# Kernel optimization log

Measured on AMD Instinct MI355X. Metric: run time of the kernel, lower is better.

## Reference

```python
import jax, jax.numpy as jnp
import numpy as np

# snntorch Leaky defaults / CFG constants
BETA = 0.9      # CFG.lif_beta
IAPP = 0.0      # CFG.Iapp
THR = 1.0       # snn.Leaky default threshold
SLOPE = 25.0    # surrogate.fast_sigmoid default slope


@jax.custom_vjp
def spike(x):
    # Heaviside spike with fast-sigmoid surrogate gradient
    return (x > 0).astype(x.dtype)

def _spike_fwd(x):
    return spike(x), x

def _spike_bwd(x, g):
    return (g / (SLOPE * jnp.abs(x) + 1.0) ** 2,)

spike.defvjp(_spike_fwd, _spike_bwd)


def setup_inputs() -> dict:
    key = jax.random.key(0)
    z = jax.random.normal(key, (32, 1024, 512), dtype=jnp.float32)
    return {"z": z}


def reference(z):
    # z: [B, T, H]; sequential LIF over time axis.
    # snntorch Leaky (reset='subtract'):
    #   reset = detach(V_prev > thr)
    #   V_k   = beta * V_prev + input_k - reset * thr
    #   spk_k = heaviside(V_k - thr)
    # Original loop: input at step k is z[:, k-1] + Iapp (noise std = 0.0).
    B, T, H = z.shape
    zt = jnp.transpose(z[:, :-1, :], (1, 0, 2))  # [T-1, B, H]
    V0 = jnp.zeros((B, H), dtype=z.dtype)

    def step(V, zin):
        reset = jax.lax.stop_gradient((V > THR).astype(V.dtype))
        Vn = BETA * V + (zin + IAPP) - reset * THR
        spk = spike(Vn - THR)
        return Vn, spk

    _, spks = jax.lax.scan(step, V0, zt)  # spks: [T-1, B, H]
    # T[:, 0, :] stays zero (loop starts at k=1)
    Tout = jnp.concatenate(
        [jnp.zeros((B, 1, H), dtype=z.dtype), jnp.transpose(spks, (1, 0, 2))],
        axis=1,
    )
    return Tout
```

## Files before the change

### kernel.cpp

```cpp
#include <hip/hip_runtime.h>


#define LIF_H 512
#define LIF_C 31

__global__ __launch_bounds__(64, 1) void lif_kernel(const float* __restrict__ z,
                                                    float* __restrict__ out) {
    const int n = blockIdx.x * 64 + threadIdx.x;
    const int b = n >> 9;
    const int h = n & (LIF_H - 1);
    const int base = b * (1024 * LIF_H) + h;

    const float* zp = z + base;
    float* op = out + base + LIF_H;

    out[base] = 0.0f;

    float bufA[LIF_C], bufB[LIF_C];
    float V = 0.0f;

#pragma unroll
    for (int i = 0; i < LIF_C; ++i) bufA[i] = zp[i * LIF_H];
    __builtin_amdgcn_sched_barrier(0);

    for (int p = 0; p < 16; ++p) {
        const int c0 = 2 * p;

#pragma unroll
        for (int i = 0; i < LIF_C; ++i)
            bufB[i] = zp[((c0 + 1) * LIF_C + i) * LIF_H];
        __builtin_amdgcn_sched_barrier(0);

#pragma unroll
        for (int i = 0; i < LIF_C; ++i) {
            const int s = c0 * LIF_C + i;
            const float v0 = __fadd_rn(__fmul_rn(0.9f, V), bufA[i]);
            const float Vn = (V > 1.0f) ? __fsub_rn(v0, 1.0f) : v0;
            op[s * LIF_H] = (Vn > 1.0f) ? 1.0f : 0.0f;
            V = Vn;
        }
        __builtin_amdgcn_sched_barrier(0);

#pragma unroll
        for (int i = 0; i < LIF_C; ++i)
            bufA[i] = zp[((c0 + 2) * LIF_C + i) * LIF_H];
        __builtin_amdgcn_sched_barrier(0);

#pragma unroll
        for (int i = 0; i < LIF_C; ++i) {
            const int s = (c0 + 1) * LIF_C + i;
            const float v0 = __fadd_rn(__fmul_rn(0.9f, V), bufB[i]);
            const float Vn = (V > 1.0f) ? __fsub_rn(v0, 1.0f) : v0;
            op[s * LIF_H] = (Vn > 1.0f) ? 1.0f : 0.0f;
            V = Vn;
        }
        __builtin_amdgcn_sched_barrier(0);
    }

#pragma unroll
    for (int i = 0; i < LIF_C; ++i) {
        const int s = 32 * LIF_C + i;
        const float v0 = __fadd_rn(__fmul_rn(0.9f, V), bufA[i]);
        const float Vn = (V > 1.0f) ? __fsub_rn(v0, 1.0f) : v0;
        op[s * LIF_H] = (Vn > 1.0f) ? 1.0f : 0.0f;
        V = Vn;
    }
}

extern "C" void kernel_launch(void* const* d_in, const int* in_sizes, int n_in,
                              void* d_out, int out_size, void* d_ws, size_t ws_size,
                              hipStream_t stream) {
    const float* z = (const float*)d_in[0];
    float* out = (float*)d_out;
    dim3 block(64);
    dim3 grid((32 * LIF_H) / 64);
    hipLaunchKernelGGL(lif_kernel, grid, block, 0, stream, z, out);
}
```

Before: 117.0 us.

## Add producer waves streaming input into double-buffered LDS via global_load_lds

Each block now has four producer waves that copy 128-timestep chunks of the input into a double-buffered LDS tile using direct global-to-LDS loads, plus one consumer wave that runs the sequential LIF recurrence from LDS. This is meant to take global-load latency off the serial dependency chain and replace strided per-lane loads with wide 16-byte loads. Block barriers at each chunk keep producers and consumer in step. The cost is a barrier per chunk and extra waves per block, while the grid stays at 256 blocks of one compute wave each.

```diff
diff --git a/kernel.cpp b/kernel.cpp
--- a/kernel.cpp
+++ b/kernel.cpp
@@ -2,68 +2,101 @@
 
 
 #define LIF_H 512
-#define LIF_C 31
+#define LIF_T 1024
+#define CH 128
+#define NCH 8
+#define NPROD 4
+#define NTHREADS (64 * (1 + NPROD))
 
-__global__ __launch_bounds__(64, 1) void lif_kernel(const float* __restrict__ z,
-                                                    float* __restrict__ out) {
-    const int n = blockIdx.x * 64 + threadIdx.x;
-    const int b = n >> 9;
-    const int h = n & (LIF_H - 1);
-    const int base = b * (1024 * LIF_H) + h;
+__global__ __launch_bounds__(NTHREADS, 1) void lif_kernel(const float* __restrict__ z,
+                                                          float* __restrict__ out) {
+    __shared__ float lds[2][CH * 64];
 
-    const float* zp = z + base;
-    float* op = out + base + LIF_H;
+    const int tid  = threadIdx.x;
+    const int wave = tid >> 6;
+    const int lane = tid & 63;
+    const int bid  = blockIdx.x;
+    const int b    = bid >> 3;
+    const int h0   = (bid & 7) << 6;
 
-    out[base] = 0.0f;
+    const float* zb = z   + b * (LIF_T * LIF_H) + h0;
+    float*       ob = out + b * (LIF_T * LIF_H) + h0;
 
-    float bufA[LIF_C], bufB[LIF_C];
+    if (wave == 0) {
+        ob[lane] = 0.0f;
+    } else {
+        const int p = wave - 1;
+#pragma unroll
+        for (int j = 0; j < 8; ++j) {
+            const int r0 = p * 32 + j * 4;
+            const float* g = zb + (r0 + (lane >> 4)) * LIF_H + (lane & 15) * 4;
+            __builtin_amdgcn_global_load_lds(
+                (__attribute__((address_space(1))) void*)g,
+                (__attribute__((address_space(3))) void*)&lds[0][r0 * 64],
+                16, 0, 0);
+        }
+        asm volatile("s_waitcnt vmcnt(0)" ::: "memory");
+    }
+    asm volatile("" ::: "memory");
+    __builtin_amdgcn_s_barrier();
+    asm volatile("" ::: "memory");
+
     float V = 0.0f;
 
+    for (int c = 0; c < NCH; ++c) {
+        const int cur = c & 1;
+
+        if (wave > 0) {
+            if (c + 1 < NCH) {
+                const int p = wave - 1;
 #pragma unroll
-    for (int i = 0; i < LIF_C; ++i) bufA[i] = zp[i * LIF_H];
-    __builtin_amdgcn_sched_barrier(0);
+                for (int j = 0; j < 8; ++j) {
+                    const int r0 = p * 32 + j * 4;
+                    const float* g = zb + ((c + 1) * CH + r0 + (lane >> 4)) * LIF_H
+                                        + (lane & 15) * 4;
+                    __builtin_amdgcn_global_load_lds(
+                        (__attribute__((address_space(1))) void*)g,
+                        (__attribute__((address_space(3))) void*)&lds[cur ^ 1][r0 * 64],
+                        16, 0, 0);
+                }
+                asm volatile("s_waitcnt vmcnt(0)" ::: "memory");
+            }
+        } else {
+            const float* lb = &lds[cur][0];
+            const bool lastc = (c == NCH - 1);
+#pragma unroll 1
+            for (int sub = 0; sub < 4; ++sub) {
+                float rb[32];
+#pragma unroll
+                for (int i = 0; i < 32; ++i)
+                    rb[i] = lb[(sub * 32 + i) * 64 + lane];
+                __builtin_amdgcn_sched_barrier(0);
 
-    for (int p = 0; p < 16; ++p) {
-        const int c0 = 2 * p;
+                const int s0 = c * CH + sub * 32;
+                if (!lastc || sub < 3) {
+#pragma unroll
+                    for (int i = 0; i < 32; ++i) {
+                        const float v0 = __fadd_rn(__fmul_rn(0.9f, V), rb[i]);
+                        const float Vn = (V > 1.0f) ? __fsub_rn(v0, 1.0f) : v0;
+                        ob[(s0 + i + 1) * LIF_H + lane] = (Vn > 1.0f) ? 1.0f : 0.0f;
+                        V = Vn;
+                    }
+                } else {
+#pragma unroll
+                    for (int i = 0; i < 31; ++i) {
+                        const float v0 = __fadd_rn(__fmul_rn(0.9f, V), rb[i]);
+                        const float Vn = (V > 1.0f) ? __fsub_rn(v0, 1.0f) : v0;
+                        ob[(s0 + i + 1) * LIF_H + lane] = (Vn > 1.0f) ? 1.0f : 0.0f;
+                        V = Vn;
+                    }
+                }
+                __builtin_amdgcn_sched_barrier(0);
+            }
+        }
 
-#pragma unroll
-        for (int i = 0; i < LIF_C; ++i)
-            bufB[i] = zp[((c0 + 1) * LIF_C + i) * LIF_H];
-        __builtin_amdgcn_sched_barrier(0);
-
-#pragma unroll
-        for (int i = 0; i < LIF_C; ++i) {
-            const int s = c0 * LIF_C + i;
-            const float v0 = __fadd_rn(__fmul_rn(0.9f, V), bufA[i]);
-            const float Vn = (V > 1.0f) ? __fsub_rn(v0, 1.0f) : v0;
-            op[s * LIF_H] = (Vn > 1.0f) ? 1.0f : 0.0f;
-            V = Vn;
-        }
-        __builtin_amdgcn_sched_barrier(0);
-
-#pragma unroll
-        for (int i = 0; i < LIF_C; ++i)
-            bufA[i] = zp[((c0 + 2) * LIF_C + i) * LIF_H];
-        __builtin_amdgcn_sched_barrier(0);
-
-#pragma unroll
-        for (int i = 0; i < LIF_C; ++i) {
-            const int s = (c0 + 1) * LIF_C + i;
-            const float v0 = __fadd_rn(__fmul_rn(0.9f, V), bufB[i]);
-            const float Vn = (V > 1.0f) ? __fsub_rn(v0, 1.0f) : v0;
-            op[s * LIF_H] = (Vn > 1.0f) ? 1.0f : 0.0f;
-            V = Vn;
-        }
-        __builtin_amdgcn_sched_barrier(0);
-    }
-
-#pragma unroll
-    for (int i = 0; i < LIF_C; ++i) {
-        const int s = 32 * LIF_C + i;
-        const float v0 = __fadd_rn(__fmul_rn(0.9f, V), bufA[i]);
-        const float Vn = (V > 1.0f) ? __fsub_rn(v0, 1.0f) : v0;
-        op[s * LIF_H] = (Vn > 1.0f) ? 1.0f : 0.0f;
-        V = Vn;
+        asm volatile("" ::: "memory");
+        __builtin_amdgcn_s_barrier();
+        asm volatile("" ::: "memory");
     }
 }
 
@@ -72,7 +105,5 @@
                               hipStream_t stream) {
     const float* z = (const float*)d_in[0];
     float* out = (float*)d_out;
-    dim3 block(64);
-    dim3 grid((32 * LIF_H) / 64);
-    hipLaunchKernelGGL(lif_kernel, grid, block, 0, stream, z, out);
+    hipLaunchKernelGGL(lif_kernel, dim3(256), dim3(NTHREADS), 0, stream, z, out);
 }
```

Measured after the change: 118.0 us. No clear change (+0.9%).
